# Kernel optimization log

Measured on AMD Instinct MI355X. Metric: run time of the kernel, lower is better.

## Reference

```python
import jax, jax.numpy as jnp
from jax import lax
import numpy as np

B, CIN, H, W_IN = 16, 1, 224, 224
COUT = 18 * 16  # 18 parallel convs, 16 channels each, fused
K = 3
HOUT, WOUT = H - K + 1, W_IN - K + 1  # VALID padding


def setup_inputs() -> dict:
    key = jax.random.key(0)
    k1, k2, k3 = jax.random.split(key, 3)
    x1 = jax.random.normal(k1, (B, CIN, H, W_IN), dtype=jnp.float32)
    W = jax.random.normal(k2, (COUT, CIN, K, K), dtype=jnp.float32)
    bias = jax.random.normal(k3, (1, COUT, HOUT, WOUT), dtype=jnp.float32)
    return {"x1": x1, "W": W, "bias": bias}


def reference(x1, W, bias):
    # Fused equivalent of 18 separate 1->16 conv2d ops + channel concat:
    # a single 1->288 VALID conv, then full-tensor bias add + ReLU epilogue.
    y = lax.conv_general_dilated(
        x1, W,
        window_strides=(1, 1),
        padding="VALID",
        dimension_numbers=("NCHW", "OIHW", "NCHW"),
    )  # (B, 288, 222, 222)
    return jax.nn.relu(y + bias)
```

## Files before the change

kernel.cpp:

```cpp
#include <hip/hip_runtime.h>


constexpr int Bn     = 16;
constexpr int COUT   = 288;
constexpr int Hin    = 224;
constexpr int Win    = 224;
constexpr int HOUT   = 222;
constexpr int WOUT   = 222;
constexpr int PLANE  = HOUT * WOUT;
constexpr int XPLANE = Hin * Win;

__global__ __launch_bounds__(256) void conv_bias_relu(
    const float* __restrict__ x,
    const float* __restrict__ wgt,
    const float* __restrict__ bias,
    float* __restrict__ out)
{
    const int tid  = threadIdx.x;
    const int lane = tid & 63;
    const int wid  = tid >> 6;

    const int c0  = blockIdx.x * 64;
    const int rb  = blockIdx.y * 16 + wid * 4;
    const int co0 = blockIdx.z * 4;

    const int  c     = c0 + lane;
    const bool colok = (c < WOUT);
    const int  ceff  = colok ? c : (WOUT - 1);

    float wt[4][9];
    #pragma unroll
    for (int q = 0; q < 4; ++q)
        #pragma unroll
        for (int k = 0; k < 9; ++k)
            wt[q][k] = wgt[(co0 + q) * 9 + k];

    int rofx[6];
    #pragma unroll
    for (int k = 0; k < 6; ++k)
        rofx[k] = min(rb + k, Hin - 1) * Win + ceff;

    bool rowok[4];
    int  rofo[4];
    #pragma unroll
    for (int p = 0; p < 4; ++p) {
        rowok[p] = (rb + p) < HOUT;
        rofo[p]  = min(rb + p, HOUT - 1) * WOUT;
    }

    float bv[4][4];
    #pragma unroll
    for (int q = 0; q < 4; ++q)
        #pragma unroll
        for (int p = 0; p < 4; ++p)
            bv[q][p] = bias[(size_t)(co0 + q) * PLANE + rofo[p] + ceff];

    for (int b = 0; b < Bn; ++b) {
        const float* xb = x + b * XPLANE;

        float xr[6][3];
        #pragma unroll
        for (int k = 0; k < 6; ++k)
            #pragma unroll
            for (int j = 0; j < 3; ++j)
                xr[k][j] = xb[rofx[k] + j];

        float acc[4][4];
        #pragma unroll
        for (int q = 0; q < 4; ++q)
            #pragma unroll
            for (int p = 0; p < 4; ++p)
                acc[q][p] = bv[q][p];

        #pragma unroll
        for (int p = 0; p < 4; ++p)
            #pragma unroll
            for (int kh = 0; kh < 3; ++kh)
                #pragma unroll
                for (int kw = 0; kw < 3; ++kw) {
                    const float xv = xr[p + kh][kw];
                    #pragma unroll
                    for (int q = 0; q < 4; ++q)
                        acc[q][p] = fmaf(wt[q][kh * 3 + kw], xv, acc[q][p]);
                }

        if (colok) {
            #pragma unroll
            for (int q = 0; q < 4; ++q) {
                float* ob = out + (size_t)(b * COUT + co0 + q) * PLANE + c;
                #pragma unroll
                for (int p = 0; p < 4; ++p)
                    if (rowok[p])
                        ob[(rb + p) * WOUT] = fmaxf(acc[q][p], 0.f);
            }
        }
    }
}

extern "C" void kernel_launch(void* const* d_in, const int* in_sizes, int n_in,
                              void* d_out, int out_size, void* d_ws, size_t ws_size,
                              hipStream_t stream) {
    const float* x    = (const float*)d_in[0];
    const float* w    = (const float*)d_in[1];
    const float* bias = (const float*)d_in[2];
    float* out        = (float*)d_out;

    dim3 block(256);
    dim3 grid((WOUT + 63) / 64,
              (HOUT + 15) / 16,
              COUT / 4);
    conv_bias_relu<<<grid, block, 0, stream>>>(x, w, bias, out);
}
```

Before: 1.154 ms.

## Flatten output plane into float4 chunks with vectorized bias, input and output access

Each thread now owns four consecutive elements of the flattened output plane (4 output channels) instead of a 4-row column strip, so the bias loads and output stores become 128-bit float4 accesses. Input rows are read as aligned float4 pairs, and a per-thread select handles the 2-element offset and the row wrap that occurs because the row width of 222 is not a multiple of 4. This aims to cut memory instruction count on a store-bound kernel. In exchange, vertical reuse of input rows across output rows is lost, and the selects add ALU work and may cost registers.

```diff
diff --git a/kernel.cpp b/kernel.cpp
--- a/kernel.cpp
+++ b/kernel.cpp
@@ -8,6 +8,7 @@
 constexpr int HOUT   = 222;
 constexpr int WOUT   = 222;
 constexpr int PLANE  = HOUT * WOUT;
+constexpr int NF4    = PLANE / 4;
 constexpr int XPLANE = Hin * Win;
 
 __global__ __launch_bounds__(256) void conv_bias_relu(
@@ -16,17 +17,21 @@
     const float* __restrict__ bias,
     float* __restrict__ out)
 {
-    const int tid  = threadIdx.x;
-    const int lane = tid & 63;
-    const int wid  = tid >> 6;
+    const int f4r    = blockIdx.x * 256 + threadIdx.x;
+    const bool active = f4r < NF4;
+    const int  f4    = active ? f4r : (NF4 - 1);
+    const int  f     = f4 * 4;
+    const int  co0   = blockIdx.y * 4;
 
-    const int c0  = blockIdx.x * 64;
-    const int rb  = blockIdx.y * 16 + wid * 4;
-    const int co0 = blockIdx.z * 4;
+    const int ho0 = f / WOUT;
+    const int wo0 = f - ho0 * WOUT;
+    const int wo0a = wo0 & ~3;
+    const int xbase = ho0 * Win + wo0a;
 
-    const int  c     = c0 + lane;
-    const bool colok = (c < WOUT);
-    const int  ceff  = colok ? c : (WOUT - 1);
+    const bool p2 = (wo0 & 2) != 0;
+    const bool cr = (wo0 == 220);
+    bool s[4];
+    s[0] = p2; s[1] = p2; s[2] = p2 || cr; s[3] = p2 || cr;
 
     float wt[4][9];
     #pragma unroll
@@ -35,63 +40,56 @@
         for (int k = 0; k < 9; ++k)
             wt[q][k] = wgt[(co0 + q) * 9 + k];
 
-    int rofx[6];
-    #pragma unroll
-    for (int k = 0; k < 6; ++k)
-        rofx[k] = min(rb + k, Hin - 1) * Win + ceff;
-
-    bool rowok[4];
-    int  rofo[4];
-    #pragma unroll
-    for (int p = 0; p < 4; ++p) {
-        rowok[p] = (rb + p) < HOUT;
-        rofo[p]  = min(rb + p, HOUT - 1) * WOUT;
-    }
-
-    float bv[4][4];
+    float4 bv[4];
     #pragma unroll
     for (int q = 0; q < 4; ++q)
-        #pragma unroll
-        for (int p = 0; p < 4; ++p)
-            bv[q][p] = bias[(size_t)(co0 + q) * PLANE + rofo[p] + ceff];
+        bv[q] = *reinterpret_cast<const float4*>(bias + (size_t)(co0 + q) * PLANE + f);
 
     for (int b = 0; b < Bn; ++b) {
-        const float* xb = x + b * XPLANE;
+        const float* xb = x + b * XPLANE + xbase;
 
-        float xr[6][3];
+        float xsp[3][8];
         #pragma unroll
-        for (int k = 0; k < 6; ++k)
-            #pragma unroll
-            for (int j = 0; j < 3; ++j)
-                xr[k][j] = xb[rofx[k] + j];
+        for (int r = 0; r < 3; ++r) {
+            const float4 a = *reinterpret_cast<const float4*>(xb + r * Win);
+            const float4 c = *reinterpret_cast<const float4*>(xb + r * Win + 4);
+            xsp[r][0] = a.x; xsp[r][1] = a.y; xsp[r][2] = a.z; xsp[r][3] = a.w;
+            xsp[r][4] = c.x; xsp[r][5] = c.y; xsp[r][6] = c.z; xsp[r][7] = c.w;
+        }
 
         float acc[4][4];
         #pragma unroll
-        for (int q = 0; q < 4; ++q)
-            #pragma unroll
-            for (int p = 0; p < 4; ++p)
-                acc[q][p] = bv[q][p];
+        for (int q = 0; q < 4; ++q) {
+            acc[q][0] = bv[q].x; acc[q][1] = bv[q].y;
+            acc[q][2] = bv[q].z; acc[q][3] = bv[q].w;
+        }
 
         #pragma unroll
-        for (int p = 0; p < 4; ++p)
+        for (int j = 0; j < 4; ++j) {
             #pragma unroll
-            for (int kh = 0; kh < 3; ++kh)
+            for (int kh = 0; kh < 3; ++kh) {
+                const float a0 = s[j] ? xsp[kh][j + 2] : xsp[kh][j + 0];
+                const float a1 = s[j] ? xsp[kh][j + 3] : xsp[kh][j + 1];
+                const float a2 = s[j] ? xsp[kh][j + 4] : xsp[kh][j + 2];
                 #pragma unroll
-                for (int kw = 0; kw < 3; ++kw) {
-                    const float xv = xr[p + kh][kw];
-                    #pragma unroll
-                    for (int q = 0; q < 4; ++q)
-                        acc[q][p] = fmaf(wt[q][kh * 3 + kw], xv, acc[q][p]);
+                for (int q = 0; q < 4; ++q) {
+                    acc[q][j] = fmaf(wt[q][kh * 3 + 0], a0, acc[q][j]);
+                    acc[q][j] = fmaf(wt[q][kh * 3 + 1], a1, acc[q][j]);
+                    acc[q][j] = fmaf(wt[q][kh * 3 + 2], a2, acc[q][j]);
                 }
+            }
+        }
 
-        if (colok) {
+        if (active) {
             #pragma unroll
             for (int q = 0; q < 4; ++q) {
-                float* ob = out + (size_t)(b * COUT + co0 + q) * PLANE + c;
-                #pragma unroll
-                for (int p = 0; p < 4; ++p)
-                    if (rowok[p])
-                        ob[(rb + p) * WOUT] = fmaxf(acc[q][p], 0.f);
+                float4 o;
+                o.x = fmaxf(acc[q][0], 0.f);
+                o.y = fmaxf(acc[q][1], 0.f);
+                o.z = fmaxf(acc[q][2], 0.f);
+                o.w = fmaxf(acc[q][3], 0.f);
+                *reinterpret_cast<float4*>(
+                    out + (size_t)(b * COUT + co0 + q) * PLANE + f) = o;
             }
         }
     }
@@ -106,8 +104,6 @@
     float* out        = (float*)d_out;
 
     dim3 block(256);
-    dim3 grid((WOUT + 63) / 64,
-              (HOUT + 15) / 16,
-              COUT / 4);
+    dim3 grid((NF4 + 255) / 256, COUT / 4);
     conv_bias_relu<<<grid, block, 0, stream>>>(x, w, bias, out);
 }
```

After: 992.6 us. 14.0% less time.
